# Optimization experiments

Hardware: AMD Instinct MI355X
Metric: run time of the kernel (lower is better)

The kernel has to match this reference:

```python
import jax, jax.numpy as jnp
import numpy as np

B, S, D, H = 4, 2048, 1024, 16
DH = D // H  # 64


def setup_inputs() -> dict:
    key = jax.random.key(0)
    ks = jax.random.split(key, 7)
    scale = 1.0 / np.sqrt(DH)  # ~ torch Linear init scale
    return {
        "seqs": jax.random.normal(ks[0], (B, S, D), dtype=jnp.float32),
        "Wq": jax.random.normal(ks[1], (H, DH, DH), dtype=jnp.float32) * scale,
        "bq": jax.random.normal(ks[2], (H, DH), dtype=jnp.float32) * scale,
        "Wk": jax.random.normal(ks[3], (H, DH, DH), dtype=jnp.float32) * scale,
        "bk": jax.random.normal(ks[4], (H, DH), dtype=jnp.float32) * scale,
        "Wv": jax.random.normal(ks[5], (H, DH, DH), dtype=jnp.float32) * scale,
        "bv": jax.random.normal(ks[6], (H, DH), dtype=jnp.float32) * scale,
    }


def reference(seqs, Wq, bq, Wk, bk, Wv, bv):
    # seqs: [B, S, D] -> per-head slices [B, S, H, DH]
    x = seqs.reshape(B, S, H, DH)
    # torch Linear: y = s @ W.T + b  (W: [out, in]) -> einsum over 'in' axis d
    q = jnp.einsum("bshd,hed->bshe", x, Wq) + bq  # [B,S,H,DH]
    k = jnp.einsum("bshd,hed->bshe", x, Wk) + bk
    v = jnp.einsum("bshd,hed->bshe", x, Wv) + bv
    inv_sqrt = 1.0 / jnp.sqrt(jnp.asarray(DH, dtype=seqs.dtype))
    scores = jnp.einsum("bshe,bthe->bhst", q, k) * inv_sqrt  # [B,H,S,S]
    attn = jax.nn.softmax(scores, axis=-1)
    out = jnp.einsum("bhst,bthe->bshe", attn, v)  # [B,S,H,DH]
    # torch.hstack over heads == concat along feature dim
    return out.reshape(B, S, D)
```

## Files before the change

### kernel.cpp

```cpp
#include <hip/hip_runtime.h>
#include <hip/hip_bf16.h>

#define NB 4
#define NS 2048
#define ND 1024
#define NH 16
#define NDH 64
#define SCF 0.18033688011112042f

typedef __attribute__((ext_vector_type(8))) short bf16x8;
typedef __attribute__((ext_vector_type(4))) float f32x4;

__device__ __forceinline__ float bf2f(unsigned short u) {
    union { unsigned int u; float f; } x; x.u = ((unsigned int)u) << 16; return x.f;
}
__device__ __forceinline__ unsigned short f2bf(float f) {
    union { float f; unsigned int u; } x; x.f = f;
    unsigned int r = x.u + 0x7FFFu + ((x.u >> 16) & 1u);
    return (unsigned short)(r >> 16);
}
__device__ __forceinline__ unsigned short f2bf_fast(float f) {
    union { float f; unsigned int u; } x; x.f = f;
    return (unsigned short)((x.u + 0x8000u) >> 16);
}
__device__ __forceinline__ unsigned int pkbf(float a, float b) {
    union { float f; unsigned int u; } x, y; x.f = a; y.f = b;
    return __builtin_amdgcn_perm(y.u + 0x8000u, x.u + 0x8000u, 0x07060302u);
}
__device__ __forceinline__ unsigned int pktr(float a, float b) {
    union { float f; unsigned int u; } x, y; x.f = a; y.f = b;
    return __builtin_amdgcn_perm(y.u, x.u, 0x07060302u);
}

__global__ __launch_bounds__(256) void convert_w_kernel(
    const unsigned short* __restrict__ x,
    const void* __restrict__ Wq, const void* __restrict__ bq,
    const void* __restrict__ Wk, const void* __restrict__ bk,
    const void* __restrict__ Wv, const void* __restrict__ bv,
    int* __restrict__ flag,
    unsigned short* __restrict__ Wb,
    unsigned short* __restrict__ Bb)
{
    __shared__ int sflag;
    const int tid = threadIdx.x;
    if (tid < 64) {
        int bad = 0, zer = 0;
        for (int i = tid; i < 1024; i += 64) {
            const unsigned short u = x[2 * i];
            const int e = (u >> 7) & 0xFF;
            if (e >= 0x8F) bad++;
            if (e == 0 && (u & 0x7F)) bad++;
            if (u == 0) zer++;
        }
        #pragma unroll
        for (int off = 1; off < 64; off <<= 1) {
            bad += __shfl_xor(bad, off, 64);
            zer += __shfl_xor(zer, off, 64);
        }
        if (tid == 0) {
            const int f = (bad > 64 || zer > 512) ? 1 : 0;
            sflag = f;
            flag[0] = f;
        }
    }
    __syncthreads();
    const int isf32 = sflag;

    const void* Wsrc[3] = { Wq, Wk, Wv };
    const void* Bsrc[3] = { bq, bk, bv };
    const int NW = 3 * 65536, NBIAS = 3 * 1024;
    for (int i = blockIdx.x * blockDim.x + tid; i < NW + NBIAS;
         i += gridDim.x * blockDim.x) {
        int m, off; const void* src; unsigned short* dst;
        if (i < NW) { m = i >> 16; off = i & 65535; src = Wsrc[m]; dst = Wb + i; }
        else { int j = i - NW; m = j >> 10; off = j & 1023; src = Bsrc[m];
               dst = Bb + j; }
        float v = isf32 ? ((const float*)src)[off]
                        : bf2f(((const unsigned short*)src)[off]);
        if (m == 0) v *= SCF;
        *dst = f2bf(v);
    }
}

__global__ __launch_bounds__(256) void qkv_proj_kernel(
    const unsigned short* __restrict__ x,
    const unsigned short* __restrict__ Wb,
    const unsigned short* __restrict__ Bb,
    const int* __restrict__ flag,
    unsigned short* __restrict__ Qw, unsigned short* __restrict__ Kw,
    unsigned short* __restrict__ VwT)
{
    __shared__ __align__(16) unsigned short Tl[3 * 64 * 72];

    const int isf32 = flag[0];
    const int tid  = threadIdx.x;
    const int wave = tid >> 6, lane = tid & 63;
    const int quad = lane >> 4, l16 = lane & 15;
    const int ttile = blockIdx.x, h = blockIdx.y;
    const int b  = ttile >> 5;
    const int s0 = (ttile & 31) * 64;
    const int bh = b * NH + h;

    const int tok_a = ttile * 64 + wave * 16 + l16;
    bf16x8 af0, af1;
    if (isf32) {
        const f32x4* xp = (const f32x4*)((const float*)x + (size_t)tok_a * ND + h * NDH);
        const f32x4 v0 = xp[quad * 2], v1 = xp[quad * 2 + 1];
        const f32x4 v2 = xp[8 + quad * 2], v3 = xp[8 + quad * 2 + 1];
        union { bf16x8 v; unsigned int d[4]; } a0, a1;
        a0.d[0] = pkbf(v0[0], v0[1]); a0.d[1] = pkbf(v0[2], v0[3]);
        a0.d[2] = pkbf(v1[0], v1[1]); a0.d[3] = pkbf(v1[2], v1[3]);
        a1.d[0] = pkbf(v2[0], v2[1]); a1.d[1] = pkbf(v2[2], v2[3]);
        a1.d[2] = pkbf(v3[0], v3[1]); a1.d[3] = pkbf(v3[2], v3[3]);
        af0 = a0.v; af1 = a1.v;
    } else {
        const unsigned short* xr = x + (size_t)tok_a * ND + h * NDH;
        af0 = *(const bf16x8*)(xr + quad * 8);
        af1 = *(const bf16x8*)(xr + 32 + quad * 8);
    }

    #pragma unroll
    for (int m = 0; m < 3; ++m) {
        const unsigned short* W = Wb + m * 65536 + h * 4096;
        unsigned short* R = Tl + m * (64 * 72);
        #pragma unroll
        for (int n = 0; n < 4; ++n) {
            const unsigned short* wrow = W + (n * 16 + l16) * NDH;
            const bf16x8 b0 = *(const bf16x8*)(wrow + quad * 8);
            const bf16x8 b1 = *(const bf16x8*)(wrow + 32 + quad * 8);
            f32x4 acc = {0.f, 0.f, 0.f, 0.f};
            acc = __builtin_amdgcn_mfma_f32_16x16x32_bf16(af0, b0, acc, 0, 0, 0);
            acc = __builtin_amdgcn_mfma_f32_16x16x32_bf16(af1, b1, acc, 0, 0, 0);
            const float bias = bf2f(Bb[m * 1024 + h * NDH + n * 16 + l16]);
            if (m < 2) {
                #pragma unroll
                for (int r = 0; r < 4; ++r) {
                    const int row = wave * 16 + quad * 4 + r;
                    R[row * 72 + n * 16 + l16] = f2bf_fast(acc[r] + bias);
                }
            } else {
                #pragma unroll
                for (int r = 0; r < 4; ++r) {
                    const int tok = wave * 16 + quad * 4 + r;
                    const int pc = ((tok & 15) << 2) | (tok >> 4);
                    R[(n * 16 + l16) * 72 + pc] = f2bf_fast(acc[r] + bias);
                }
            }
        }
    }
    __syncthreads();
    #pragma unroll
    for (int p = 0; p < 2; ++p) {
        const int ch = tid + p * 256;
        const int tl = ch >> 3, sub = ch & 7;
        *(bf16x8*)(Qw + ((size_t)bh * NS + s0 + tl) * NDH + sub * 8) =
            *(const bf16x8*)(Tl + tl * 72 + sub * 8);
        *(bf16x8*)(Kw + ((size_t)bh * NS + s0 + tl) * NDH + sub * 8) =
            *(const bf16x8*)(Tl + 64 * 72 + tl * 72 + sub * 8);
        *(bf16x8*)(VwT + ((size_t)bh * NDH + tl) * NS + s0 + sub * 8) =
            *(const bf16x8*)(Tl + 2 * 64 * 72 + tl * 72 + sub * 8);
    }
}

__global__ __launch_bounds__(256, 2) void attn_kernel(
    const unsigned short* __restrict__ Qw,
    const unsigned short* __restrict__ Kw,
    const unsigned short* __restrict__ VwT,
    const int* __restrict__ flag,
    unsigned short* __restrict__ out)
{
    __shared__ __align__(16) unsigned short smem[5 * 64 * 72];
    unsigned short* Pt = smem + 4 * 64 * 72;
    unsigned short* Ot = smem;

    const int isf32 = flag[0];
    const int tid  = threadIdx.x;
    const int wave = tid >> 6, lane = tid & 63;
    const int quad = lane >> 4, l16 = lane & 15;
    const int qt = blockIdx.x & 7;
    const int bh = blockIdx.x >> 3;
    const int b = bh >> 4, h = bh & 15;

    const unsigned short* Qb = Qw  + (size_t)bh * NS * NDH;
    const unsigned short* Kb = Kw  + (size_t)bh * NS * NDH;
    const unsigned short* Vb = VwT + (size_t)bh * NDH * NS;

    bf16x8 qf[4][2];
    #pragma unroll
    for (int mh = 0; mh < 4; ++mh) {
        const int tok = qt * 256 + wave * 64 + mh * 16 + l16;
        qf[mh][0] = *(const bf16x8*)(Qb + (size_t)tok * NDH + quad * 8);
        qf[mh][1] = *(const bf16x8*)(Qb + (size_t)tok * NDH + 32 + quad * 8);
    }

    f32x4 o[4][4];
    float os[4][4];
    #pragma unroll
    for (int mh = 0; mh < 4; ++mh) {
        #pragma unroll
        for (int n = 0; n < 4; ++n) o[mh][n] = f32x4{0.f, 0.f, 0.f, 0.f};
        #pragma unroll
        for (int r = 0; r < 4; ++r) os[mh][r] = 0.f;
    }

    const int stage_r = tid >> 3, stage_c = tid & 7;
    unsigned short* PtW = Pt + wave * (16 * 72);

    bf16x8 kpre[2], vpre[2];
    #pragma unroll
    for (int p = 0; p < 2; ++p) {
        const int rr = stage_r + p * 32;
        kpre[p] = *(const bf16x8*)(Kb + (size_t)rr * NDH + stage_c * 8);
        vpre[p] = *(const bf16x8*)(Vb + (size_t)rr * NS + stage_c * 8);
    }

    for (int kt = 0; kt < NS / 64; ++kt) {
        unsigned short* KB = smem + (kt & 1) * (64 * 72);
        unsigned short* VB = smem + (2 + (kt & 1)) * (64 * 72);
        #pragma unroll
        for (int p = 0; p < 2; ++p) {
            const int rr = stage_r + p * 32;
            *(bf16x8*)(KB + rr * 72 + stage_c * 8) = kpre[p];
            *(bf16x8*)(VB + rr * 72 + stage_c * 8) = vpre[p];
        }
        __syncthreads();
        if (kt + 1 < NS / 64) {
            #pragma unroll
            for (int p = 0; p < 2; ++p) {
                const int rr = stage_r + p * 32;
                kpre[p] = *(const bf16x8*)(Kb + (size_t)((kt + 1) * 64 + rr) * NDH + stage_c * 8);
                vpre[p] = *(const bf16x8*)(Vb + (size_t)rr * NS + (kt + 1) * 64 + stage_c * 8);
            }
        }

        bf16x8 kb[4][2], vb[4][2];
        #pragma unroll
        for (int n = 0; n < 4; ++n) {
            kb[n][0] = *(const bf16x8*)(KB + (n * 16 + l16) * 72 + quad * 8);
            kb[n][1] = *(const bf16x8*)(KB + (n * 16 + l16) * 72 + 32 + quad * 8);
            vb[n][0] = *(const bf16x8*)(VB + (n * 16 + l16) * 72 + quad * 8);
            vb[n][1] = *(const bf16x8*)(VB + (n * 16 + l16) * 72 + 32 + quad * 8);
        }

        #pragma unroll
        for (int mh = 0; mh < 4; ++mh) {
            f32x4 sf[4];
            #pragma unroll
            for (int n = 0; n < 4; ++n) {
                f32x4 acc = {0.f, 0.f, 0.f, 0.f};
                acc = __builtin_amdgcn_mfma_f32_16x16x32_bf16(qf[mh][0], kb[n][0], acc, 0, 0, 0);
                acc = __builtin_amdgcn_mfma_f32_16x16x32_bf16(qf[mh][1], kb[n][1], acc, 0, 0, 0);
                sf[n] = acc;
            }
            #pragma unroll
            for (int r = 0; r < 4; ++r) {
                const float p0 = __builtin_amdgcn_exp2f(sf[0][r]);
                const float p1 = __builtin_amdgcn_exp2f(sf[1][r]);
                const float p2 = __builtin_amdgcn_exp2f(sf[2][r]);
                const float p3 = __builtin_amdgcn_exp2f(sf[3][r]);
                os[mh][r] += (p0 + p1) + (p2 + p3);
                uint2 d; d.x = pktr(p0, p1); d.y = pktr(p2, p3);
                *(uint2*)(PtW + (quad * 4 + r) * 72 + l16 * 4) = d;
            }
            const bf16x8 pa0 = *(const bf16x8*)(PtW + l16 * 72 + quad * 8);
            const bf16x8 pa1 = *(const bf16x8*)(PtW + l16 * 72 + 32 + quad * 8);
            #pragma unroll
            for (int n = 0; n < 4; ++n) {
                o[mh][n] = __builtin_amdgcn_mfma_f32_16x16x32_bf16(pa0, vb[n][0], o[mh][n], 0, 0, 0);
                o[mh][n] = __builtin_amdgcn_mfma_f32_16x16x32_bf16(pa1, vb[n][1], o[mh][n], 0, 0, 0);
            }
        }
    }

    float inv[4][4];
    #pragma unroll
    for (int mh = 0; mh < 4; ++mh) {
        #pragma unroll
        for (int r = 0; r < 4; ++r) {
            float s = os[mh][r];
            #pragma unroll
            for (int off = 1; off < 16; off <<= 1)
                s += __shfl_xor(s, off, 64);
            inv[mh][r] = 1.0f / s;
        }
    }

    if (isf32) {
        float* of = (float*)out;
        #pragma unroll
        for (int mh = 0; mh < 4; ++mh) {
            #pragma unroll
            for (int r = 0; r < 4; ++r) {
                const int s = qt * 256 + wave * 64 + mh * 16 + quad * 4 + r;
                #pragma unroll
                for (int n = 0; n < 4; ++n)
                    of[((size_t)(b * NS + s)) * ND + h * NDH + n * 16 + l16] =
                        o[mh][n][r] * inv[mh][r];
            }
        }
    } else {
        __syncthreads();
        #pragma unroll
        for (int mh = 0; mh < 4; ++mh) {
            #pragma unroll
            for (int r = 0; r < 4; ++r) {
                const int row = wave * 64 + mh * 16 + quad * 4 + r;
                #pragma unroll
                for (int n = 0; n < 4; ++n)
                    Ot[row * 72 + n * 16 + l16] = f2bf(o[mh][n][r] * inv[mh][r]);
            }
        }
        __syncthreads();
        #pragma unroll
        for (int p = 0; p < 8; ++p) {
            const int ch = tid + p * 256;
            const int tl = ch >> 3, sub = ch & 7;
            const int s = qt * 256 + tl;
            *(bf16x8*)(out + ((size_t)(b * NS + s)) * ND + h * NDH + sub * 8) =
                *(const bf16x8*)(Ot + tl * 72 + sub * 8);
        }
    }
}

extern "C" void kernel_launch(void* const* d_in, const int* in_sizes, int n_in,
                              void* d_out, int out_size, void* d_ws, size_t ws_size,
                              hipStream_t stream)
{
    const unsigned short* x = (const unsigned short*)d_in[0];
    int* flag = (int*)d_ws;
    const size_t per = (size_t)NB * NH * NS * NDH;
    unsigned short* Qw  = (unsigned short*)((char*)d_ws + 256);
    unsigned short* Kw  = Qw + per;
    unsigned short* VwT = Kw + per;
    unsigned short* Wb  = VwT + per;
    unsigned short* Bb  = Wb + 3 * 65536;

    convert_w_kernel<<<256, 256, 0, stream>>>(
        x, d_in[1], d_in[2], d_in[3], d_in[4], d_in[5], d_in[6], flag, Wb, Bb);
    qkv_proj_kernel<<<dim3(NB * NS / 64, NH), 256, 0, stream>>>(
        x, Wb, Bb, flag, Qw, Kw, VwT);
    attn_kernel<<<NB * NH * (NS / 256), 256, 0, stream>>>(
        Qw, Kw, VwT, flag, (unsigned short*)d_out);
}
```

Baseline: 197.2 us.

## Load K/V fragments directly from global memory, dropping shared-memory staging and barriers

Removes the cooperative double-buffered shared-memory staging of K and V tiles and the per-tile __syncthreads. Each wave now loads its MFMA K and V fragments straight from global memory (relying on L2/L1 reuse across blocks), prefetching the next K tile in registers between the QK and PV phases. The P scratch grows to a full 64x64 per-wave tile so all four row groups are written before the PV MFMAs. Block indexing is also swapped so consecutive blocks belong to different heads. The trade is more global and cache traffic and exposed load latency in exchange for no barriers and no LDS copies.

```diff
diff --git a/kernel.cpp b/kernel.cpp
--- a/kernel.cpp
+++ b/kernel.cpp
@@ -169,16 +169,16 @@
     const int* __restrict__ flag,
     unsigned short* __restrict__ out)
 {
-    __shared__ __align__(16) unsigned short smem[5 * 64 * 72];
-    unsigned short* Pt = smem + 4 * 64 * 72;
+    __shared__ __align__(16) unsigned short smem[4 * 64 * 72];
+    unsigned short* Pt = smem;
     unsigned short* Ot = smem;
 
     const int isf32 = flag[0];
     const int tid  = threadIdx.x;
     const int wave = tid >> 6, lane = tid & 63;
     const int quad = lane >> 4, l16 = lane & 15;
-    const int qt = blockIdx.x & 7;
-    const int bh = blockIdx.x >> 3;
+    const int bh = blockIdx.x & 63;
+    const int qt = blockIdx.x >> 6;
     const int b = bh >> 4, h = bh & 15;
 
     const unsigned short* Qb = Qw  + (size_t)bh * NS * NDH;
@@ -203,43 +203,24 @@
         for (int r = 0; r < 4; ++r) os[mh][r] = 0.f;
     }
 
-    const int stage_r = tid >> 3, stage_c = tid & 7;
-    unsigned short* PtW = Pt + wave * (16 * 72);
-
-    bf16x8 kpre[2], vpre[2];
-    #pragma unroll
-    for (int p = 0; p < 2; ++p) {
-        const int rr = stage_r + p * 32;
-        kpre[p] = *(const bf16x8*)(Kb + (size_t)rr * NDH + stage_c * 8);
-        vpre[p] = *(const bf16x8*)(Vb + (size_t)rr * NS + stage_c * 8);
+    unsigned short* PtW = Pt + wave * (64 * 72);
+
+    bf16x8 kb[4][2];
+    #pragma unroll
+    for (int n = 0; n < 4; ++n) {
+        const unsigned short* kr = Kb + (size_t)(n * 16 + l16) * NDH + quad * 8;
+        kb[n][0] = *(const bf16x8*)(kr);
+        kb[n][1] = *(const bf16x8*)(kr + 32);
     }
 
     for (int kt = 0; kt < NS / 64; ++kt) {
-        unsigned short* KB = smem + (kt & 1) * (64 * 72);
-        unsigned short* VB = smem + (2 + (kt & 1)) * (64 * 72);
-        #pragma unroll
-        for (int p = 0; p < 2; ++p) {
-            const int rr = stage_r + p * 32;
-            *(bf16x8*)(KB + rr * 72 + stage_c * 8) = kpre[p];
-            *(bf16x8*)(VB + rr * 72 + stage_c * 8) = vpre[p];
-        }
-        __syncthreads();
-        if (kt + 1 < NS / 64) {
-            #pragma unroll
-            for (int p = 0; p < 2; ++p) {
-                const int rr = stage_r + p * 32;
-                kpre[p] = *(const bf16x8*)(Kb + (size_t)((kt + 1) * 64 + rr) * NDH + stage_c * 8);
-                vpre[p] = *(const bf16x8*)(Vb + (size_t)rr * NS + (kt + 1) * 64 + stage_c * 8);
-            }
-        }
-
-        bf16x8 kb[4][2], vb[4][2];
+        bf16x8 vb[4][2];
         #pragma unroll
         for (int n = 0; n < 4; ++n) {
-            kb[n][0] = *(const bf16x8*)(KB + (n * 16 + l16) * 72 + quad * 8);
-            kb[n][1] = *(const bf16x8*)(KB + (n * 16 + l16) * 72 + 32 + quad * 8);
-            vb[n][0] = *(const bf16x8*)(VB + (n * 16 + l16) * 72 + quad * 8);
-            vb[n][1] = *(const bf16x8*)(VB + (n * 16 + l16) * 72 + 32 + quad * 8);
+            const unsigned short* vr = Vb + (size_t)(n * 16 + l16) * NS
+                                       + kt * 64 + quad * 8;
+            vb[n][0] = *(const bf16x8*)(vr);
+            vb[n][1] = *(const bf16x8*)(vr + 32);
         }
 
         #pragma unroll
@@ -260,10 +241,25 @@
                 const float p3 = __builtin_amdgcn_exp2f(sf[3][r]);
                 os[mh][r] += (p0 + p1) + (p2 + p3);
                 uint2 d; d.x = pktr(p0, p1); d.y = pktr(p2, p3);
-                *(uint2*)(PtW + (quad * 4 + r) * 72 + l16 * 4) = d;
-            }
-            const bf16x8 pa0 = *(const bf16x8*)(PtW + l16 * 72 + quad * 8);
-            const bf16x8 pa1 = *(const bf16x8*)(PtW + l16 * 72 + 32 + quad * 8);
+                *(uint2*)(PtW + (mh * 16 + quad * 4 + r) * 72 + l16 * 4) = d;
+            }
+        }
+
+        {
+            const int ktn = (kt + 1) & (NS / 64 - 1);
+            #pragma unroll
+            for (int n = 0; n < 4; ++n) {
+                const unsigned short* kr = Kb + (size_t)(ktn * 64 + n * 16 + l16) * NDH
+                                           + quad * 8;
+                kb[n][0] = *(const bf16x8*)(kr);
+                kb[n][1] = *(const bf16x8*)(kr + 32);
+            }
+        }
+
+        #pragma unroll
+        for (int mh = 0; mh < 4; ++mh) {
+            const bf16x8 pa0 = *(const bf16x8*)(PtW + (mh * 16 + l16) * 72 + quad * 8);
+            const bf16x8 pa1 = *(const bf16x8*)(PtW + (mh * 16 + l16) * 72 + 32 + quad * 8);
             #pragma unroll
             for (int n = 0; n < 4; ++n) {
                 o[mh][n] = __builtin_amdgcn_mfma_f32_16x16x32_bf16(pa0, vb[n][0], o[mh][n], 0, 0, 0);
```

New measurement: 245.9 us. +24.7%, slower.

## Split attention over two key halves with a separate combine kernel

Applied to the files above, without the earlier changes.

The attention kernel now splits the key sequence in two, doubling the grid from 512 to 1024 blocks. Each block writes unnormalized partial outputs in bf16 and partial row sums to workspace, and a new combine kernel adds the halves and normalizes. Shared memory drops to single-buffered K/V tiles with an extra barrier per iteration, and launch bounds rise to 4 blocks per SM to raise occupancy. The cost is an extra kernel launch, extra global traffic for the partials, and another bf16 rounding of those partials. There is no running max, because the softmax has none and relies on score magnitudes staying small.

```diff
diff --git a/kernel.cpp b/kernel.cpp
--- a/kernel.cpp
+++ b/kernel.cpp
@@ -162,24 +162,25 @@
     }
 }
 
-__global__ __launch_bounds__(256, 2) void attn_kernel(
+__global__ __launch_bounds__(256, 4) void attn_kernel(
     const unsigned short* __restrict__ Qw,
     const unsigned short* __restrict__ Kw,
     const unsigned short* __restrict__ VwT,
-    const int* __restrict__ flag,
-    unsigned short* __restrict__ out)
-{
-    __shared__ __align__(16) unsigned short smem[5 * 64 * 72];
-    unsigned short* Pt = smem + 4 * 64 * 72;
-    unsigned short* Ot = smem;
-
-    const int isf32 = flag[0];
+    unsigned short* __restrict__ Opart,
+    float* __restrict__ lpart)
+{
+    __shared__ __align__(16) unsigned short smem[3 * 64 * 72];
+    unsigned short* KB = smem;
+    unsigned short* VB = smem + 64 * 72;
+    unsigned short* Pt = smem + 2 * 64 * 72;
+
     const int tid  = threadIdx.x;
     const int wave = tid >> 6, lane = tid & 63;
     const int quad = lane >> 4, l16 = lane & 15;
-    const int qt = blockIdx.x & 7;
-    const int bh = blockIdx.x >> 3;
-    const int b = bh >> 4, h = bh & 15;
+    const int bh = blockIdx.x & 63;
+    const int qt = (blockIdx.x >> 6) & 7;
+    const int ks = blockIdx.x >> 9;
+    const int k0 = ks * (NS / 2);
 
     const unsigned short* Qb = Qw  + (size_t)bh * NS * NDH;
     const unsigned short* Kb = Kw  + (size_t)bh * NS * NDH;
@@ -210,13 +211,12 @@
     #pragma unroll
     for (int p = 0; p < 2; ++p) {
         const int rr = stage_r + p * 32;
-        kpre[p] = *(const bf16x8*)(Kb + (size_t)rr * NDH + stage_c * 8);
-        vpre[p] = *(const bf16x8*)(Vb + (size_t)rr * NS + stage_c * 8);
-    }
-
-    for (int kt = 0; kt < NS / 64; ++kt) {
-        unsigned short* KB = smem + (kt & 1) * (64 * 72);
-        unsigned short* VB = smem + (2 + (kt & 1)) * (64 * 72);
+        kpre[p] = *(const bf16x8*)(Kb + (size_t)(k0 + rr) * NDH + stage_c * 8);
+        vpre[p] = *(const bf16x8*)(Vb + (size_t)rr * NS + k0 + stage_c * 8);
+    }
+
+    for (int kt = 0; kt < NS / 2 / 64; ++kt) {
+        __syncthreads();
         #pragma unroll
         for (int p = 0; p < 2; ++p) {
             const int rr = stage_r + p * 32;
@@ -224,12 +224,12 @@
             *(bf16x8*)(VB + rr * 72 + stage_c * 8) = vpre[p];
         }
         __syncthreads();
-        if (kt + 1 < NS / 64) {
+        if (kt + 1 < NS / 2 / 64) {
             #pragma unroll
             for (int p = 0; p < 2; ++p) {
                 const int rr = stage_r + p * 32;
-                kpre[p] = *(const bf16x8*)(Kb + (size_t)((kt + 1) * 64 + rr) * NDH + stage_c * 8);
-                vpre[p] = *(const bf16x8*)(Vb + (size_t)rr * NS + (kt + 1) * 64 + stage_c * 8);
+                kpre[p] = *(const bf16x8*)(Kb + (size_t)(k0 + (kt + 1) * 64 + rr) * NDH + stage_c * 8);
+                vpre[p] = *(const bf16x8*)(Vb + (size_t)rr * NS + k0 + (kt + 1) * 64 + stage_c * 8);
             }
         }
 
@@ -272,7 +272,7 @@
         }
     }
 
-    float inv[4][4];
+    const int s0w = qt * 256 + wave * 64;
     #pragma unroll
     for (int mh = 0; mh < 4; ++mh) {
         #pragma unroll
@@ -281,44 +281,63 @@
             #pragma unroll
             for (int off = 1; off < 16; off <<= 1)
                 s += __shfl_xor(s, off, 64);
-            inv[mh][r] = 1.0f / s;
-        }
-    }
-
-    if (isf32) {
+            if (l16 == 0)
+                lpart[(size_t)ks * 64 * NS + bh * NS + s0w + mh * 16 + quad * 4 + r] = s;
+        }
+    }
+
+    unsigned short* Ob = Opart + ((size_t)ks * 64 + bh) * NS * NDH;
+    #pragma unroll
+    for (int mh = 0; mh < 4; ++mh) {
+        #pragma unroll
+        for (int r = 0; r < 4; ++r)
+            #pragma unroll
+            for (int n = 0; n < 4; ++n)
+                PtW[(quad * 4 + r) * 72 + n * 16 + l16] = f2bf(o[mh][n][r]);
+        const int row = lane >> 2;
+        #pragma unroll
+        for (int p = 0; p < 2; ++p) {
+            const int chunk = (lane & 3) + p * 4;
+            *(bf16x8*)(Ob + (size_t)(s0w + mh * 16 + row) * NDH + chunk * 8) =
+                *(const bf16x8*)(PtW + row * 72 + chunk * 8);
+        }
+    }
+}
+
+__global__ __launch_bounds__(256) void combine_kernel(
+    const unsigned short* __restrict__ Opart,
+    const float* __restrict__ lpart,
+    const int* __restrict__ flag,
+    unsigned short* __restrict__ out)
+{
+    const int idx = blockIdx.x * 256 + threadIdx.x;
+    const int e8 = idx & 7;
+    const int s  = (idx >> 3) & (NS - 1);
+    const int bh = idx >> 14;
+    const int b = bh >> 4, h = bh & 15;
+
+    const size_t o0 = ((size_t)bh * NS + s) * NDH + e8 * 8;
+    const size_t o1 = o0 + (size_t)64 * NS * NDH;
+    const bf16x8 a = *(const bf16x8*)(Opart + o0);
+    const bf16x8 c = *(const bf16x8*)(Opart + o1);
+    const float inv = 1.0f / (lpart[bh * NS + s] + lpart[64 * NS + bh * NS + s]);
+
+    float v[8];
+    #pragma unroll
+    for (int j = 0; j < 8; ++j)
+        v[j] = (bf2f((unsigned short)a[j]) + bf2f((unsigned short)c[j])) * inv;
+
+    const size_t ob = ((size_t)b * NS + s) * ND + h * NDH + e8 * 8;
+    if (flag[0]) {
         float* of = (float*)out;
-        #pragma unroll
-        for (int mh = 0; mh < 4; ++mh) {
-            #pragma unroll
-            for (int r = 0; r < 4; ++r) {
-                const int s = qt * 256 + wave * 64 + mh * 16 + quad * 4 + r;
-                #pragma unroll
-                for (int n = 0; n < 4; ++n)
-                    of[((size_t)(b * NS + s)) * ND + h * NDH + n * 16 + l16] =
-                        o[mh][n][r] * inv[mh][r];
-            }
-        }
+        f32x4 w0 = {v[0], v[1], v[2], v[3]}, w1 = {v[4], v[5], v[6], v[7]};
+        *(f32x4*)(of + ob) = w0;
+        *(f32x4*)(of + ob + 4) = w1;
     } else {
-        __syncthreads();
-        #pragma unroll
-        for (int mh = 0; mh < 4; ++mh) {
-            #pragma unroll
-            for (int r = 0; r < 4; ++r) {
-                const int row = wave * 64 + mh * 16 + quad * 4 + r;
-                #pragma unroll
-                for (int n = 0; n < 4; ++n)
-                    Ot[row * 72 + n * 16 + l16] = f2bf(o[mh][n][r] * inv[mh][r]);
-            }
-        }
-        __syncthreads();
-        #pragma unroll
-        for (int p = 0; p < 8; ++p) {
-            const int ch = tid + p * 256;
-            const int tl = ch >> 3, sub = ch & 7;
-            const int s = qt * 256 + tl;
-            *(bf16x8*)(out + ((size_t)(b * NS + s)) * ND + h * NDH + sub * 8) =
-                *(const bf16x8*)(Ot + tl * 72 + sub * 8);
-        }
+        bf16x8 w;
+        #pragma unroll
+        for (int j = 0; j < 8; ++j) w[j] = (short)f2bf(v[j]);
+        *(bf16x8*)(out + ob) = w;
     }
 }
 
@@ -329,16 +348,19 @@
     const unsigned short* x = (const unsigned short*)d_in[0];
     int* flag = (int*)d_ws;
     const size_t per = (size_t)NB * NH * NS * NDH;
-    unsigned short* Qw  = (unsigned short*)((char*)d_ws + 256);
-    unsigned short* Kw  = Qw + per;
-    unsigned short* VwT = Kw + per;
-    unsigned short* Wb  = VwT + per;
-    unsigned short* Bb  = Wb + 3 * 65536;
+    unsigned short* Qw    = (unsigned short*)((char*)d_ws + 256);
+    unsigned short* Kw    = Qw + per;
+    unsigned short* VwT   = Kw + per;
+    unsigned short* Wb    = VwT + per;
+    unsigned short* Bb    = Wb + 3 * 65536;
+    unsigned short* Opart = Bb + 3 * 1024;
+    float*          lpart = (float*)(Opart + 2 * per);
 
     convert_w_kernel<<<256, 256, 0, stream>>>(
         x, d_in[1], d_in[2], d_in[3], d_in[4], d_in[5], d_in[6], flag, Wb, Bb);
     qkv_proj_kernel<<<dim3(NB * NS / 64, NH), 256, 0, stream>>>(
         x, Wb, Bb, flag, Qw, Kw, VwT);
-    attn_kernel<<<NB * NH * (NS / 256), 256, 0, stream>>>(
-        Qw, Kw, VwT, flag, (unsigned short*)d_out);
-}
+    attn_kernel<<<1024, 256, 0, stream>>>(Qw, Kw, VwT, Opart, lpart);
+    combine_kernel<<<4096, 256, 0, stream>>>(Opart, lpart, flag,
+                                             (unsigned short*)d_out);
+}
```

Result: slower. 582.5 us (+195.3%).
